# Kernel optimization log

Measured on AMD Instinct MI355X. Metric: run time of the kernel, lower is better.

The kernel has to match this reference:

```python
import jax, jax.numpy as jnp
import numpy as np

COLOR_SIZE = 4
SIZE = 64
FILTERS = 512
LENGTH = SIZE * SIZE * 3  # 12288


def setup_inputs() -> dict:
    key = jax.random.key(0)
    k1, k2, k3 = jax.random.split(key, 3)
    example = jax.random.randint(k1, (8, SIZE, SIZE, 3), 0, COLOR_SIZE, dtype=jnp.int32)
    kernel = jax.random.normal(k2, (FILTERS, LENGTH), dtype=jnp.float32)
    bias = jnp.zeros((FILTERS,), dtype=jnp.float32)
    dense_w = jax.random.normal(k3, (FILTERS, COLOR_SIZE), dtype=jnp.float32) * 0.02
    dense_b = jnp.zeros((COLOR_SIZE,), dtype=jnp.float32)
    return {"example": example, "kernel": kernel, "bias": bias,
            "dense_w": dense_w, "dense_b": dense_b}


def reference(example, kernel, bias, dense_w, dense_b):
    B = example.shape[0]
    L = kernel.shape[1]  # 12288
    # normalize int pixels to [-1, 1)
    x = example.astype(jnp.float32) / COLOR_SIZE * 2.0 - 1.0
    x = x.reshape(B, L)                                   # [B, L]
    # FFT-based long (causal full) convolution, fft_length = 2L
    Xf = jnp.fft.rfft(x, n=2 * L, axis=-1)                # [B, L+1] complex64
    Kf = jnp.fft.rfft(kernel, n=2 * L, axis=-1)           # [F, L+1]
    y = jnp.fft.irfft(Xf[:, None, :] * Kf[None, :, :], n=2 * L, axis=-1)[..., :L]  # [B, F, L]
    y = jnp.transpose(y, (0, 2, 1)) + bias                # [B, L, F]
    y = jax.nn.relu(y)
    out = y @ dense_w + dense_b                           # [B, L, color_size]
    return out.reshape(B, SIZE, SIZE, 3, COLOR_SIZE).astype(jnp.float32)
```

## Files before the change

kernel.cpp:

```cpp
#include <hip/hip_runtime.h>

#define FF 512
#define LL 12288
#define NJC 1556
#define NR 128

typedef _Float16 half8  __attribute__((ext_vector_type(8)));
typedef float    f32x16 __attribute__((ext_vector_type(16)));

__global__ __launch_bounds__(256) void build_At(const float* __restrict__ kern,
                                                _Float16* __restrict__ At) {
    int tid  = blockIdx.x * 256 + threadIdx.x;
    int lane = tid & 63;
    int rest = tid >> 6;
    int kc   = rest % 768;
    int ft   = rest / 768;
    int f    = ft * 32 + (lane & 31);
    int d0   = kc * 16 + (lane >> 5) * 8;
    const float* src = kern + (size_t)f * LL + d0;
    half8 v;
#pragma unroll
    for (int i = 0; i < 8; ++i) v[i] = (_Float16)src[i];
    ((half8*)At)[tid] = v;
}

__global__ __launch_bounds__(256) void build_XB(const int* __restrict__ ex,
                                                _Float16* __restrict__ XB) {
    int tid = blockIdx.x * 256 + threadIdx.x;
    if (tid >= NJC * NR) return;
    int r  = tid & 127;
    int jc = tid >> 7;
    int s  = r >> 3, b = r & 7;
    int j0 = jc * 8;
    half8 v;
#pragma unroll
    for (int i = 0; i < 8; ++i) {
        int idx = LL - 1 - (j0 + i) - s;
        float x = 0.f;
        if (idx >= 0) x = (float)ex[b * LL + idx] * 0.5f - 1.0f;
        v[i] = (_Float16)x;
    }
    ((half8*)XB)[tid] = v;
}

__global__ __launch_bounds__(256) void init_out(const float* __restrict__ db,
                                                float* __restrict__ out) {
    int tid = blockIdx.x * 256 + threadIdx.x;
    out[tid] = db[tid & 3];
}

__device__ __forceinline__ void gl_lds16(const half8* g, half8* l) {
    __builtin_amdgcn_global_load_lds((const __attribute__((address_space(1))) void*)g,
                                     (__attribute__((address_space(3))) void*)l, 16, 0, 0);
}

__global__ __launch_bounds__(256, 2) void conv_main(const _Float16* __restrict__ At,
                                                    const _Float16* __restrict__ XB,
                                                    const float* __restrict__ bias,
                                                    const float* __restrict__ dw,
                                                    float* __restrict__ out) {
    __shared__ half8 Abuf[2][8][4][64];

    int bx    = blockIdx.x;
    int slot  = bx & 7;
    int f_blk = slot >> 1;
    int n_blk = 383 - ((bx >> 3) * 2 + (slot & 1));
    int n0 = n_blk << 5;
    int S  = n_blk + 1;
    int M  = (S + 3) >> 2;

    int tid  = threadIdx.x;
    int lane = tid & 63;
    int wid  = tid >> 6;
    int kh   = lane >> 5;
    int bb   = lane & 7;
    int nh   = (lane >> 3) & 3;

    const half8* Ag = (const half8*)At;
    const half8* ag = Ag + ((size_t)(f_blk * 4 + wid) * 768) * 64 + lane;

    const half8* Bg = (const half8*)XB;
    const half8* pB[2];
#pragma unroll
    for (int ti = 0; ti < 2; ++ti) {
        int n_base = n0 + (wid * 2 + ti) * 4;
        int Qt = LL - 1 - n_base - nh;
        int s  = Qt & 7;
        int jc0 = Qt >> 3;
        pB[ti] = Bg + (size_t)(jc0 + kh) * 128 + s * 8 + bb;
    }

    f32x16 acc[4][2];
#pragma unroll
    for (int mt = 0; mt < 4; ++mt)
#pragma unroll
        for (int ti = 0; ti < 2; ++ti)
#pragma unroll
            for (int r = 0; r < 16; ++r) acc[mt][ti][r] = 0.f;

#pragma unroll
    for (int kc = 0; kc < 8; ++kc)
        gl_lds16(ag + (size_t)kc * 64, &Abuf[0][kc][wid][lane]);
    half8 bf[2][2][2];
#pragma unroll
    for (int ti = 0; ti < 2; ++ti) {
        bf[0][0][ti] = pB[ti][0];
        bf[0][1][ti] = pB[ti][256];
    }
    __syncthreads();

    for (int mc = 0; mc < M; ++mc) {
        int buf = mc & 1;
        if (mc + 1 < M) {
            size_t oa = (size_t)(mc + 1) * 512;
#pragma unroll
            for (int kc = 0; kc < 8; ++kc)
                gl_lds16(ag + oa + (size_t)kc * 64, &Abuf[buf ^ 1][kc][wid][lane]);
        }
#pragma unroll
        for (int d4 = 0; d4 < 4; ++d4) {
            int dcg = mc * 4 + d4;
            int p   = dcg & 1;
            size_t ob = (size_t)(dcg + 1) * 512;
#pragma unroll
            for (int ti = 0; ti < 2; ++ti) {
                bf[p ^ 1][0][ti] = pB[ti][ob];
                bf[p ^ 1][1][ti] = pB[ti][ob + 256];
            }
            half8 a0[4], a1[4];
#pragma unroll
            for (int mt = 0; mt < 4; ++mt) {
                a0[mt] = Abuf[buf][d4 * 2][mt][lane];
                a1[mt] = Abuf[buf][d4 * 2 + 1][mt][lane];
            }
#pragma unroll
            for (int mt = 0; mt < 4; ++mt)
#pragma unroll
                for (int ti = 0; ti < 2; ++ti)
                    acc[mt][ti] = __builtin_amdgcn_mfma_f32_32x32x16_f16(a0[mt], bf[p][0][ti], acc[mt][ti], 0, 0, 0);
#pragma unroll
            for (int mt = 0; mt < 4; ++mt)
#pragma unroll
                for (int ti = 0; ti < 2; ++ti)
                    acc[mt][ti] = __builtin_amdgcn_mfma_f32_32x32x16_f16(a1[mt], bf[p][1][ti], acc[mt][ti], 0, 0, 0);
        }
        __syncthreads();
    }

    float p[2][4] = {{0.f}};
#pragma unroll
    for (int mt = 0; mt < 4; ++mt) {
#pragma unroll
        for (int reg = 0; reg < 16; ++reg) {
            int row = (reg & 3) + 8 * (reg >> 2) + 4 * kh;
            int f   = f_blk * 128 + mt * 32 + row;
            float bs = bias[f];
            float4 w = *(const float4*)(dw + (size_t)f * 4);
#pragma unroll
            for (int ti = 0; ti < 2; ++ti) {
                float y = fmaxf(acc[mt][ti][reg] + bs, 0.f);
                p[ti][0] += y * w.x; p[ti][1] += y * w.y;
                p[ti][2] += y * w.z; p[ti][3] += y * w.w;
            }
        }
    }
#pragma unroll
    for (int ti = 0; ti < 2; ++ti)
#pragma unroll
        for (int c = 0; c < 4; ++c) {
            float v = p[ti][c];
            v += __shfl_xor(v, 32, 64);
            p[ti][c] = v;
        }
    if (kh == 0) {
#pragma unroll
        for (int ti = 0; ti < 2; ++ti) {
            int n = n0 + (wid * 2 + ti) * 4 + nh;
            float* o = out + ((size_t)bb * LL + n) * 4;
#pragma unroll
            for (int c = 0; c < 4; ++c) atomicAdd(o + c, p[ti][c]);
        }
    }
}

extern "C" void kernel_launch(void* const* d_in, const int* in_sizes, int n_in,
                              void* d_out, int out_size, void* d_ws, size_t ws_size,
                              hipStream_t stream) {
    const int*   ex   = (const int*)d_in[0];
    const float* kern = (const float*)d_in[1];
    const float* bias = (const float*)d_in[2];
    const float* dw   = (const float*)d_in[3];
    const float* db   = (const float*)d_in[4];
    float* out = (float*)d_out;

    _Float16* At = (_Float16*)d_ws;
    _Float16* XB = (_Float16*)((char*)d_ws + (size_t)FF * LL * 2);

    hipLaunchKernelGGL(build_At, dim3(3072), dim3(256), 0, stream, kern, At);
    hipLaunchKernelGGL(build_XB, dim3(778),  dim3(256), 0, stream, ex, XB);
    hipLaunchKernelGGL(init_out, dim3(1536), dim3(256), 0, stream, db, out);
    hipLaunchKernelGGL(conv_main, dim3(1536), dim3(256), 0, stream, At, XB, bias, dw, out);
}
```

Baseline: 550.0 us.

## Load A fragments directly from global into registers, dropping LDS staging

Removes the LDS double-buffer and its per-chunk __syncthreads. Each wave now loads all four A tiles straight from global memory into registers, with a two-stage register prefetch. This removes barrier and LDS traffic, but every wave now re-reads the A tiles that were previously loaded once per block and shared. That raises global/L2 traffic and register pressure. The loop bound also changes from rounded-up chunks of 8 k-steps to exactly 2*(n_blk+1) k-steps, which trims wasted MFMA work on the causal boundary.

```diff
diff --git a/kernel.cpp b/kernel.cpp
--- a/kernel.cpp
+++ b/kernel.cpp
@@ -49,25 +49,17 @@
     out[tid] = db[tid & 3];
 }
 
-__device__ __forceinline__ void gl_lds16(const half8* g, half8* l) {
-    __builtin_amdgcn_global_load_lds((const __attribute__((address_space(1))) void*)g,
-                                     (__attribute__((address_space(3))) void*)l, 16, 0, 0);
-}
-
 __global__ __launch_bounds__(256, 2) void conv_main(const _Float16* __restrict__ At,
                                                     const _Float16* __restrict__ XB,
                                                     const float* __restrict__ bias,
                                                     const float* __restrict__ dw,
                                                     float* __restrict__ out) {
-    __shared__ half8 Abuf[2][8][4][64];
-
     int bx    = blockIdx.x;
     int slot  = bx & 7;
     int f_blk = slot >> 1;
     int n_blk = 383 - ((bx >> 3) * 2 + (slot & 1));
     int n0 = n_blk << 5;
-    int S  = n_blk + 1;
-    int M  = (S + 3) >> 2;
+    int T  = 2 * (n_blk + 1);
 
     int tid  = threadIdx.x;
     int lane = tid & 63;
@@ -77,7 +69,10 @@
     int nh   = (lane >> 3) & 3;
 
     const half8* Ag = (const half8*)At;
-    const half8* ag = Ag + ((size_t)(f_blk * 4 + wid) * 768) * 64 + lane;
+    const half8* pAm[4];
+#pragma unroll
+    for (int mt = 0; mt < 4; ++mt)
+        pAm[mt] = Ag + ((size_t)(f_blk * 4 + mt) * 768) * 64 + lane;
 
     const half8* Bg = (const half8*)XB;
     const half8* pB[2];
@@ -98,53 +93,33 @@
 #pragma unroll
             for (int r = 0; r < 16; ++r) acc[mt][ti][r] = 0.f;
 
+    half8 a[2][4], b[2][2];
 #pragma unroll
-    for (int kc = 0; kc < 8; ++kc)
-        gl_lds16(ag + (size_t)kc * 64, &Abuf[0][kc][wid][lane]);
-    half8 bf[2][2][2];
+    for (int mt = 0; mt < 4; ++mt) a[0][mt] = pAm[mt][0];
 #pragma unroll
-    for (int ti = 0; ti < 2; ++ti) {
-        bf[0][0][ti] = pB[ti][0];
-        bf[0][1][ti] = pB[ti][256];
-    }
-    __syncthreads();
+    for (int ti = 0; ti < 2; ++ti) b[0][ti] = pB[ti][0];
 
-    for (int mc = 0; mc < M; ++mc) {
-        int buf = mc & 1;
-        if (mc + 1 < M) {
-            size_t oa = (size_t)(mc + 1) * 512;
+    for (int kk = 0; kk < T; kk += 2) {
+        size_t o1 = (size_t)(kk + 1);
 #pragma unroll
-            for (int kc = 0; kc < 8; ++kc)
-                gl_lds16(ag + oa + (size_t)kc * 64, &Abuf[buf ^ 1][kc][wid][lane]);
-        }
+        for (int mt = 0; mt < 4; ++mt) a[1][mt] = pAm[mt][o1 * 64];
 #pragma unroll
-        for (int d4 = 0; d4 < 4; ++d4) {
-            int dcg = mc * 4 + d4;
-            int p   = dcg & 1;
-            size_t ob = (size_t)(dcg + 1) * 512;
+        for (int ti = 0; ti < 2; ++ti) b[1][ti] = pB[ti][o1 * 256];
 #pragma unroll
-            for (int ti = 0; ti < 2; ++ti) {
-                bf[p ^ 1][0][ti] = pB[ti][ob];
-                bf[p ^ 1][1][ti] = pB[ti][ob + 256];
-            }
-            half8 a0[4], a1[4];
+        for (int mt = 0; mt < 4; ++mt)
 #pragma unroll
-            for (int mt = 0; mt < 4; ++mt) {
-                a0[mt] = Abuf[buf][d4 * 2][mt][lane];
-                a1[mt] = Abuf[buf][d4 * 2 + 1][mt][lane];
-            }
+            for (int ti = 0; ti < 2; ++ti)
+                acc[mt][ti] = __builtin_amdgcn_mfma_f32_32x32x16_f16(a[0][mt], b[0][ti], acc[mt][ti], 0, 0, 0);
+        size_t o2 = (size_t)(kk + 2);
 #pragma unroll
-            for (int mt = 0; mt < 4; ++mt)
+        for (int mt = 0; mt < 4; ++mt) a[0][mt] = pAm[mt][o2 * 64];
 #pragma unroll
-                for (int ti = 0; ti < 2; ++ti)
-                    acc[mt][ti] = __builtin_amdgcn_mfma_f32_32x32x16_f16(a0[mt], bf[p][0][ti], acc[mt][ti], 0, 0, 0);
+        for (int ti = 0; ti < 2; ++ti) b[0][ti] = pB[ti][o2 * 256];
 #pragma unroll
-            for (int mt = 0; mt < 4; ++mt)
+        for (int mt = 0; mt < 4; ++mt)
 #pragma unroll
-                for (int ti = 0; ti < 2; ++ti)
-                    acc[mt][ti] = __builtin_amdgcn_mfma_f32_32x32x16_f16(a1[mt], bf[p][1][ti], acc[mt][ti], 0, 0, 0);
-        }
-        __syncthreads();
+            for (int ti = 0; ti < 2; ++ti)
+                acc[mt][ti] = __builtin_amdgcn_mfma_f32_32x32x16_f16(a[1][mt], b[1][ti], acc[mt][ti], 0, 0, 0);
     }
 
     float p[2][4] = {{0.f}};
```

Result: slower. 762.1 us (+38.5%).
